# Optimization experiments

Measured on AMD Instinct MI355X. Metric: run time of the kernel, lower is better.

Reference implementation:

```python
import jax, jax.numpy as jnp
from jax import lax
import numpy as np


def _hsig(x):
    # Keras hard_sigmoid (default recurrent_activation of ConvLSTM2D)
    return jnp.clip(0.2 * x + 0.5, 0.0, 1.0)


def _conv(x, k):
    return lax.conv_general_dilated(x, k, (1, 1), 'SAME',
                                    dimension_numbers=('NHWC', 'HWIO', 'NHWC'))


def _convlstm(x, W, U, b, return_seq=True):
    # x: [B,T,H,W,Cin]; W: [kh,kw,Cin,4C]; U: [kh,kw,C,4C]; b: [4C]
    B, T, H, Wd, Ci = x.shape
    C = b.shape[0] // 4
    # input-to-gate convs for all timesteps at once (batched over B*T)
    xz = _conv(x.reshape(B * T, H, Wd, Ci), W).reshape(B, T, H, Wd, 4 * C) + b

    def step(carry, z_t):
        h, c = carry
        z = z_t + _conv(h, U)
        zi, zf, zc, zo = jnp.split(z, 4, axis=-1)  # Keras gate order i,f,c,o
        c = _hsig(zf) * c + _hsig(zi) * jax.nn.relu(zc)  # activation='relu'
        h = _hsig(zo) * jax.nn.relu(c)
        return (h, c), h

    h0 = jnp.zeros((B, H, Wd, C), x.dtype)
    (hT, _), hs = lax.scan(step, (h0, h0), jnp.swapaxes(xz, 0, 1))
    return jnp.swapaxes(hs, 0, 1) if return_seq else hT


def _pool(x):  # MaxPooling3D(pool_size=(1,2,2)) on [B,T,H,W,C]
    return lax.reduce_window(x, -jnp.inf, lax.max,
                             (1, 1, 2, 2, 1), (1, 1, 2, 2, 1), 'VALID')


def _up(x):  # UpSampling3D(size=(1,2,2))
    return jnp.repeat(jnp.repeat(x, 2, axis=2), 2, axis=3)


def _forward(x, w1a, u1a, b1a, w1b, u1b, b1b, w2a, u2a, b2a, w2b, u2b, b2b,
             w3a, u3a, b3a, w3b, u3b, b3b, w4a, u4a, b4a, w4b, u4b, b4b,
             w5a, u5a, b5a, w5b, u5b, b5b, w6a, u6a, b6a, w6b, u6b, b6b,
             w7a, u7a, b7a, w7b, u7b, b7b, wout, uout, bout):
    c1 = _convlstm(_convlstm(x, w1a, u1a, b1a), w1b, u1b, b1b)
    c2 = _convlstm(_convlstm(_pool(c1), w2a, u2a, b2a), w2b, u2b, b2b)
    c3 = _convlstm(_convlstm(_pool(c2), w3a, u3a, b3a), w3b, u3b, b3b)
    c4 = _convlstm(_convlstm(_pool(c3), w4a, u4a, b4a), w4b, u4b, b4b)
    m5 = jnp.concatenate([c3, _up(c4)], axis=-1)
    c5 = _convlstm(_convlstm(m5, w5a, u5a, b5a), w5b, u5b, b5b)
    m6 = jnp.concatenate([c2, _up(c5)], axis=-1)
    c6 = _convlstm(_convlstm(m6, w6a, u6a, b6a), w6b, u6b, b6b)
    m7 = jnp.concatenate([c1, _up(c6)], axis=-1)
    c7 = _convlstm(_convlstm(m7, w7a, u7a, b7a), w7b, u7b, b7b)
    return _convlstm(c7, wout, uout, bout, return_seq=False)  # [B,H,W,1]


def setup_inputs() -> dict:
    key = jax.random.key(0)
    keys = iter(jax.random.split(key, 64))

    def p(*s):
        return jax.random.normal(next(keys), s, jnp.float32) * 0.05

    d = {'x': jax.random.normal(next(keys), (1, 4, 256, 256, 1), jnp.float32)}
    specs = [('1a', 1, 32), ('1b', 32, 32), ('2a', 32, 64), ('2b', 64, 64),
             ('3a', 64, 128), ('3b', 128, 128), ('4a', 128, 256), ('4b', 256, 256),
             ('5a', 384, 128), ('5b', 128, 128), ('6a', 192, 64), ('6b', 64, 64),
             ('7a', 96, 32), ('7b', 32, 32)]
    for n, ci, co in specs:
        d['w' + n] = p(3, 3, ci, 4 * co)
        d['u' + n] = p(3, 3, co, 4 * co)
        d['b' + n] = jnp.zeros((4 * co,), jnp.float32)
    d['wout'] = p(1, 1, 32, 4)
    d['uout'] = p(1, 1, 1, 4)
    d['bout'] = jnp.zeros((4,), jnp.float32)
    return d


def reference(x, w1a, u1a, b1a, w1b, u1b, b1b, w2a, u2a, b2a, w2b, u2b, b2b,
              w3a, u3a, b3a, w3b, u3b, b3b, w4a, u4a, b4a, w4b, u4b, b4b,
              w5a, u5a, b5a, w5b, u5b, b5b, w6a, u6a, b6a, w6b, u6b, b6b,
              w7a, u7a, b7a, w7b, u7b, b7b, wout, uout, bout):
    return _forward(x, w1a, u1a, b1a, w1b, u1b, b1b, w2a, u2a, b2a, w2b, u2b, b2b,
                    w3a, u3a, b3a, w3b, u3b, b3b, w4a, u4a, b4a, w4b, u4b, b4b,
                    w5a, u5a, b5a, w5b, u5b, b5b, w6a, u6a, b6a, w6b, u6b, b6b,
                    w7a, u7a, b7a, w7b, u7b, b7b, wout, uout, bout)
```

## Files before the change

kernel.cpp:

```cpp
#include <hip/hip_runtime.h>
#include <hip/hip_bf16.h>

#define T_STEPS 4

typedef __attribute__((ext_vector_type(8))) short short8v;
typedef __attribute__((ext_vector_type(4))) float f32x4;
typedef __attribute__((ext_vector_type(4))) unsigned short us4;

__device__ __forceinline__ float hsig(float x) {
    return fminf(fmaxf(0.2f * x + 0.5f, 0.f), 1.f);
}
__device__ __forceinline__ unsigned short f2bf(float v) {
    __hip_bfloat16 h = __float2bfloat16(v);
    unsigned short u; __builtin_memcpy(&u, &h, 2); return u;
}

template<int TILE>
__global__ __launch_bounds__(256, (TILE == 16) ? 3 : 6)
void lstm_mfma(const float* __restrict__ xin, const float* __restrict__ hprev,
               float* __restrict__ cst, float* __restrict__ hout,
               const unsigned short* __restrict__ BtX,
               const unsigned short* __restrict__ BtH,
               const float* __restrict__ bias,
               int H, int W, int CiR, int CiP, int C)
{
    constexpr int HS = TILE + 2;
    constexpr int PITCH = 40;
    constexpr int NSLOT = HS * HS * 8;
    constexpr int NFM = (TILE == 16) ? 4 : 2;
    constexpr int NN  = (TILE == 16) ? 4 : 2;
    extern __shared__ char smem[];
    unsigned short* ldsA = (unsigned short*)smem;

    const int tid = threadIdx.x, w = tid >> 6, lane = tid & 63;
    const int nb = blockIdx.z;
    const int y0 = blockIdx.y * TILE, x0 = blockIdx.x * TILE;
    const int NG = (4 * C) >> 4;
    const int kq = lane >> 4;

    int abase;
    if (TILE == 16) abase = (w * 4) * HS * PITCH + (lane & 15) * PITCH + kq * 8;
    else abase = ((w >> 1) * 4 + ((lane >> 3) & 1)) * HS * PITCH + (lane & 7) * PITCH + kq * 8;

    f32x4 acc[NFM][NN];
#pragma unroll
    for (int a = 0; a < NFM; ++a)
#pragma unroll
        for (int b = 0; b < NN; ++b) acc[a][b] = (f32x4)0.f;

    for (int s = 0; s < 2; ++s) {
        if (s == 1 && hprev == nullptr) break;
        const float* __restrict__ src = s ? hprev : xin;
        const int CsR = s ? C : CiR;
        const int CsP = s ? C : CiP;
        const unsigned short* __restrict__ Bt = s ? BtH : BtX;
        const int nch = CsP >> 5;

        for (int ck = 0; ck < nch; ++ck) {
            __syncthreads();
            const int ci0 = ck << 5;
            for (int i = tid; i < NSLOT; i += 256) {
                const int pix = i >> 3, c4 = (i & 7) << 2;
                const int hy = pix / HS, hx = pix - hy * HS;
                const int iy = y0 + hy - 1, ix = x0 + hx - 1;
                float4 v = make_float4(0.f, 0.f, 0.f, 0.f);
                if (iy >= 0 && iy < H && ix >= 0 && ix < W) {
                    const float* gp = src + ((size_t)iy * W + ix) * CsR + ci0 + c4;
                    if (ci0 + c4 + 4 <= CsR) v = *(const float4*)gp;
                    else {
                        const int rem = CsR - ci0 - c4;
                        if (rem > 0) { v.x = gp[0]; if (rem > 1) v.y = gp[1]; if (rem > 2) v.z = gp[2]; }
                    }
                }
                us4 hi;
                hi[0] = f2bf(v.x); hi[1] = f2bf(v.y);
                hi[2] = f2bf(v.z); hi[3] = f2bf(v.w);
                *(us4*)(ldsA + pix * PITCH + c4) = hi;
            }
            short8v bcur[NN], bnxt[NN];
#pragma unroll
            for (int nn = 0; nn < NN; ++nn) {
                const int ng = (TILE == 16) ? nn : ((w & 1) * 2 + nn);
                bcur[nn] = *(const short8v*)(Bt +
                    ((size_t)((ck * 9) * NG + nb * 4 + ng) << 9) + lane * 8);
            }
            __syncthreads();
#pragma unroll
            for (int dd = 0; dd < 9; ++dd) {
                if (dd < 8) {
#pragma unroll
                    for (int nn = 0; nn < NN; ++nn) {
                        const int ng = (TILE == 16) ? nn : ((w & 1) * 2 + nn);
                        bnxt[nn] = *(const short8v*)(Bt +
                            ((size_t)((ck * 9 + dd + 1) * NG + nb * 4 + ng) << 9) + lane * 8);
                    }
                }
                const int dy = dd / 3, dx = dd % 3;
                short8v ah[NFM];
#pragma unroll
                for (int fm = 0; fm < NFM; ++fm) {
                    const int ro = (TILE == 16) ? (fm + dy) : (2 * fm + dy);
                    ah[fm] = *(const short8v*)(ldsA + abase + (ro * HS + dx) * PITCH);
                }
#pragma unroll
                for (int nn = 0; nn < NN; ++nn)
#pragma unroll
                    for (int fm = 0; fm < NFM; ++fm)
                        acc[fm][nn] = __builtin_amdgcn_mfma_f32_16x16x32_bf16(ah[fm], bcur[nn], acc[fm][nn], 0, 0, 0);
                if (dd < 8) {
#pragma unroll
                    for (int nn = 0; nn < NN; ++nn) bcur[nn] = bnxt[nn];
                }
            }
        }
    }

    __syncthreads();
    float* lds2 = (float*)smem + w * 276;
    const int rr = lane & 15, cl = lane >> 4;
#pragma unroll
    for (int nn = 0; nn < NN; ++nn) {
        const int ngl = (TILE == 16) ? nn : ((w & 1) * 2 + nn);
        const int c = nb * 16 + ngl * 4 + cl;
        float b4[4];
#pragma unroll
        for (int g = 0; g < 4; ++g) b4[g] = bias[g * C + c];
#pragma unroll
        for (int fm = 0; fm < NFM; ++fm) {
#pragma unroll
            for (int j = 0; j < 4; ++j) lds2[(cl * 4 + j) * 17 + rr] = acc[fm][nn][j];
            float z[4];
#pragma unroll
            for (int g = 0; g < 4; ++g) z[g] = lds2[rr * 17 + cl * 4 + g];
            int py, px;
            if (TILE == 16) { py = y0 + w * 4 + fm; px = x0 + rr; }
            else { py = y0 + (w >> 1) * 4 + 2 * fm + (rr >> 3); px = x0 + (rr & 7); }
            const size_t base = ((size_t)py * W + px) * C + c;
            const float cold = hprev ? cst[base] : 0.f;
            const float zi = z[0] + b4[0], zf = z[1] + b4[1];
            const float zc = z[2] + b4[2], zo = z[3] + b4[3];
            const float cn = hsig(zf) * cold + hsig(zi) * fmaxf(zc, 0.f);
            const float hv = hsig(zo) * fmaxf(cn, 0.f);
            cst[base] = cn; hout[base] = hv;
        }
    }
}

__global__ void transform_w_kernel(const float* __restrict__ Wsrc,
                                   unsigned short* __restrict__ Bt,
                                   int CsR, int C, int total)
{
    const int i = blockIdx.x * 256 + threadIdx.x;
    if (i >= total) return;
    const int N = 4 * C, NG = N >> 4;
    const int lane = i & 63; int t = i >> 6;
    const int ng = t % NG; t /= NG;
    const int dd = t % 9; const int ck = t / 9;
    const int colp = ng * 16 + (lane & 15);
    const int c = colp >> 2, g = colp & 3, co = g * C + c;
    const int kb = (lane >> 4) * 8;
    short8v hi8;
#pragma unroll
    for (int e = 0; e < 8; ++e) {
        const int ci = (ck << 5) + kb + e;
        const float v = (ci < CsR) ? Wsrc[(size_t)(dd * CsR + ci) * N + co] : 0.f;
        hi8[e] = (short)f2bf(v);
    }
    const size_t base = ((size_t)(ck * 9 + dd) * NG + ng) * 512 + lane * 8;
    *(short8v*)(Bt + base) = hi8;
}

__global__ void pool_kernel(const float* __restrict__ in, float* __restrict__ out,
                            int H, int Wd, int C, long total4)
{
    const int Ho = H >> 1, Wo = Wd >> 1;
    const int C4 = C >> 2;
    for (long i = (long)blockIdx.x * blockDim.x + threadIdx.x; i < total4;
         i += (long)gridDim.x * blockDim.x) {
        const int c4 = (int)(i % C4);
        long r = i / C4;
        const int x = (int)(r % Wo); r /= Wo;
        const int y = (int)(r % Ho);
        const int t = (int)(r / Ho);
        const float4* a = reinterpret_cast<const float4*>(in) +
                          (((long)t * H + 2 * y) * Wd + 2 * x) * C4 + c4;
        const float4 v00 = a[0], v01 = a[C4];
        const float4 v10 = a[(long)Wd * C4], v11 = a[(long)Wd * C4 + C4];
        float4 o;
        o.x = fmaxf(fmaxf(v00.x, v01.x), fmaxf(v10.x, v11.x));
        o.y = fmaxf(fmaxf(v00.y, v01.y), fmaxf(v10.y, v11.y));
        o.z = fmaxf(fmaxf(v00.z, v01.z), fmaxf(v10.z, v11.z));
        o.w = fmaxf(fmaxf(v00.w, v01.w), fmaxf(v10.w, v11.w));
        reinterpret_cast<float4*>(out)[i] = o;
    }
}

__global__ void upconcat_kernel(const float* __restrict__ A, const float* __restrict__ B,
                                float* __restrict__ out, int H, int Wd, int C1, int C2,
                                long total4)
{
    const int Co4 = (C1 + C2) >> 2, C14 = C1 >> 2, C24 = C2 >> 2;
    for (long i = (long)blockIdx.x * blockDim.x + threadIdx.x; i < total4;
         i += (long)gridDim.x * blockDim.x) {
        const int c4 = (int)(i % Co4);
        long r = i / Co4;
        const int x = (int)(r % Wd); r /= Wd;
        const int y = (int)(r % H);
        const int t = (int)(r / H);
        float4 v;
        if (c4 < C14)
            v = reinterpret_cast<const float4*>(A)[(((long)t * H + y) * Wd + x) * C14 + c4];
        else
            v = reinterpret_cast<const float4*>(B)[
                (((long)t * (H >> 1) + (y >> 1)) * (Wd >> 1) + (x >> 1)) * C24 + (c4 - C14)];
        reinterpret_cast<float4*>(out)[i] = v;
    }
}

__global__ void final_step_kernel(const float* __restrict__ h7, const float* __restrict__ hprev,
                                  float* __restrict__ cst, float* __restrict__ hout,
                                  const float* __restrict__ wout,
                                  const float* __restrict__ uout,
                                  const float* __restrict__ bout,
                                  float* __restrict__ dout, int N)
{
    const int i = blockIdx.x * 256 + threadIdx.x;
    if (i >= N) return;
    float z0 = bout[0], z1 = bout[1], z2 = bout[2], z3 = bout[3];
    const float* hp = h7 + (size_t)i * 32;
#pragma unroll
    for (int c = 0; c < 32; c += 4) {
        const float4 h4 = *reinterpret_cast<const float4*>(hp + c);
        const float hv4[4] = {h4.x, h4.y, h4.z, h4.w};
#pragma unroll
        for (int j = 0; j < 4; ++j) {
            z0 += hv4[j] * wout[(c + j) * 4 + 0];
            z1 += hv4[j] * wout[(c + j) * 4 + 1];
            z2 += hv4[j] * wout[(c + j) * 4 + 2];
            z3 += hv4[j] * wout[(c + j) * 4 + 3];
        }
    }
    float hpv = 0.f, cold = 0.f;
    if (hprev) { hpv = hprev[i]; cold = cst[i]; }
    z0 += hpv * uout[0]; z1 += hpv * uout[1]; z2 += hpv * uout[2]; z3 += hpv * uout[3];
    const float ig = hsig(z0), fg = hsig(z1), og = hsig(z3);
    const float cd = fmaxf(z2, 0.f);
    const float cn = fg * cold + ig * cd;
    const float hv = og * fmaxf(cn, 0.f);
    cst[i] = cn; hout[i] = hv;
    if (dout) dout[i] = hv;
}

struct LD { int H, W, CiR, CiP, C, tile, wi; };

static void run_layer(const LD& L, const float* in, float* out, float* cstate,
                      const unsigned short* btx, const unsigned short* bth,
                      const float* bias, hipStream_t stream)
{
    const size_t inS = (size_t)L.H * L.W * L.CiR, outS = (size_t)L.H * L.W * L.C;
    const dim3 grid(L.W / L.tile, L.H / L.tile, (4 * L.C) / 64);
    for (int t = 0; t < T_STEPS; ++t) {
        const float* hp = t ? out + (t - 1) * outS : nullptr;
        if (L.tile == 16) {
            const size_t sh = (size_t)18 * 18 * 40 * 2;
            lstm_mfma<16><<<grid, 256, sh, stream>>>(in + t * inS, hp, cstate, out + t * outS,
                                                     btx, bth, bias, L.H, L.W, L.CiR, L.CiP, L.C);
        } else {
            const size_t sh = (size_t)10 * 10 * 40 * 2;
            lstm_mfma<8><<<grid, 256, sh, stream>>>(in + t * inS, hp, cstate, out + t * outS,
                                                    btx, bth, bias, L.H, L.W, L.CiR, L.CiP, L.C);
        }
    }
}

extern "C" void kernel_launch(void* const* d_in, const int* in_sizes, int n_in,
                              void* d_out, int out_size, void* d_ws, size_t ws_size,
                              hipStream_t stream)
{
    (void)in_sizes; (void)n_in; (void)out_size; (void)ws_size;
    const float* x = (const float*)d_in[0];
    auto Wp = [&](int k) { return (const float*)d_in[k]; };
    char* ws = (char*)d_ws;
    const size_t MiB = 1ull << 20;
    auto f = [&](size_t m) { return (float*)(ws + m * MiB); };

    hipFuncSetAttribute((const void*)lstm_mfma<16>,
                        hipFuncAttributeMaxDynamicSharedMemorySize, 26624);
    hipFuncSetAttribute((const void*)lstm_mfma<8>,
                        hipFuncAttributeMaxDynamicSharedMemorySize, 8192);

    float* bC1  = f(0);    float* bC2  = f(32);  float* bC3  = f(48);
    float* bCST = f(56);
    float* bHF  = (float*)(ws + 64 * MiB);
    float* bCF  = (float*)(ws + 64 * MiB + 256 * 1024);
    float* bS1A = f(65);   float* bP1  = f(97);  float* bS2A = f(105);
    float* bP2  = f(97);   float* bS3A = f(101); float* bP3  = f(65);
    float* bS4A = f(67);   float* bC4  = f(71);  float* bM5  = f(75);
    float* bS5A = f(99);   float* bC5  = f(65);  float* bM6  = f(73);
    float* bS6A = f(121);  float* bC6  = f(65);  float* bM7  = f(81);
    float* bS7A = f(0);    float* bC7  = f(81);

    static const LD Ls[14] = {
        {256, 256,   1,  32,  32, 16,  1}, {256, 256,  32,  32,  32, 16,  4},
        {128, 128,  32,  32,  64,  8,  7}, {128, 128,  64,  64,  64,  8, 10},
        { 64,  64,  64,  64, 128,  8, 13}, { 64,  64, 128, 128, 128,  8, 16},
        { 32,  32, 128, 128, 256,  8, 19}, { 32,  32, 256, 256, 256,  8, 22},
        { 64,  64, 384, 384, 128,  8, 25}, { 64,  64, 128, 128, 128,  8, 28},
        {128, 128, 192, 192,  64,  8, 31}, {128, 128,  64,  64,  64,  8, 34},
        {256, 256,  96,  96,  32, 16, 37}, {256, 256,  32,  32,  32, 16, 40},
    };

    unsigned short* btx[14]; unsigned short* bth[14];
    {
        size_t cur = 177 * MiB;
        for (int i = 0; i < 14; ++i) {
            const LD& L = Ls[i];
            const int NG = (4 * L.C) >> 4;
            const size_t szx = (size_t)(L.CiP >> 5) * 9 * NG * 1024;
            const size_t szh = (size_t)(L.C  >> 5) * 9 * NG * 1024;
            btx[i] = (unsigned short*)(ws + cur); cur += szx;
            bth[i] = (unsigned short*)(ws + cur); cur += szh;
            const int totx = (L.CiP >> 5) * 9 * NG * 64;
            const int toth = (L.C  >> 5) * 9 * NG * 64;
            transform_w_kernel<<<(totx + 255) / 256, 256, 0, stream>>>(
                Wp(L.wi), btx[i], L.CiR, L.C, totx);
            transform_w_kernel<<<(toth + 255) / 256, 256, 0, stream>>>(
                Wp(L.wi + 1), bth[i], L.C, L.C, toth);
        }
    }

    auto pool = [&](const float* in, float* out, int H, int Wd, int C) {
        long total4 = (long)T_STEPS * (H / 2) * (Wd / 2) * (C / 4);
        long nb = (total4 + 255) / 256; if (nb > 4096) nb = 4096;
        pool_kernel<<<dim3((unsigned)nb), 256, 0, stream>>>(in, out, H, Wd, C, total4);
    };
    auto upcat = [&](const float* A, const float* B, float* out, int H, int Wd, int C1, int C2) {
        long total4 = (long)T_STEPS * H * Wd * ((C1 + C2) / 4);
        long nb = (total4 + 255) / 256; if (nb > 8192) nb = 8192;
        upconcat_kernel<<<dim3((unsigned)nb), 256, 0, stream>>>(A, B, out, H, Wd, C1, C2, total4);
    };
    auto run = [&](int i, const float* in, float* out) {
        run_layer(Ls[i], in, out, bCST, btx[i], bth[i], Wp(Ls[i].wi + 2), stream);
    };

    run(0, x, bS1A);        run(1, bS1A, bC1);
    pool(bC1, bP1, 256, 256, 32);
    run(2, bP1, bS2A);      run(3, bS2A, bC2);
    pool(bC2, bP2, 128, 128, 64);
    run(4, bP2, bS3A);      run(5, bS3A, bC3);
    pool(bC3, bP3, 64, 64, 128);
    run(6, bP3, bS4A);      run(7, bS4A, bC4);
    upcat(bC3, bC4, bM5, 64, 64, 128, 256);
    run(8, bM5, bS5A);      run(9, bS5A, bC5);
    upcat(bC2, bC5, bM6, 128, 128, 64, 128);
    run(10, bM6, bS6A);     run(11, bS6A, bC6);
    upcat(bC1, bC6, bM7, 256, 256, 32, 64);
    run(12, bM7, bS7A);     run(13, bS7A, bC7);

    const int N = 256 * 256;
    for (int t = 0; t < T_STEPS; ++t) {
        const float* h7 = bC7 + (size_t)t * N * 32;
        final_step_kernel<<<N / 256, 256, 0, stream>>>(
            h7, t ? bHF : nullptr, bCF, bHF, Wp(43), Wp(44), Wp(45),
            (t == T_STEPS - 1) ? (float*)d_out : nullptr, N);
    }
}
```

Baseline: 2.146 ms.

## Prefetch next input chunk into registers during MFMA loop; batch weight transforms

The main ConvLSTM kernel now merges the x and h channel-chunk loops into one loop. It issues the global loads for the next chunk into registers before running the current chunk's MFMAs, so load latency overlaps with compute. The LDS store only converts the staged values to bf16. This costs extra registers, so the launch-bounds occupancy targets are lowered. The 28 separate weight-transform launches are also combined into a single 2D-grid launch to cut launch overhead.

```diff
diff --git a/kernel.cpp b/kernel.cpp
--- a/kernel.cpp
+++ b/kernel.cpp
@@ -16,7 +16,7 @@
 }
 
 template<int TILE>
-__global__ __launch_bounds__(256, (TILE == 16) ? 3 : 6)
+__global__ __launch_bounds__(256, (TILE == 16) ? 2 : 4)
 void lstm_mfma(const float* __restrict__ xin, const float* __restrict__ hprev,
                float* __restrict__ cst, float* __restrict__ hout,
                const unsigned short* __restrict__ BtX,
@@ -27,6 +27,7 @@
     constexpr int HS = TILE + 2;
     constexpr int PITCH = 40;
     constexpr int NSLOT = HS * HS * 8;
+    constexpr int ITERS = (NSLOT + 255) / 256;
     constexpr int NFM = (TILE == 16) ? 4 : 2;
     constexpr int NN  = (TILE == 16) ? 4 : 2;
     extern __shared__ char smem[];
@@ -48,22 +49,23 @@
 #pragma unroll
         for (int b = 0; b < NN; ++b) acc[a][b] = (f32x4)0.f;
 
-    for (int s = 0; s < 2; ++s) {
-        if (s == 1 && hprev == nullptr) break;
-        const float* __restrict__ src = s ? hprev : xin;
-        const int CsR = s ? C : CiR;
-        const int CsP = s ? C : CiP;
-        const unsigned short* __restrict__ Bt = s ? BtH : BtX;
-        const int nch = CsP >> 5;
-
-        for (int ck = 0; ck < nch; ++ck) {
-            __syncthreads();
-            const int ci0 = ck << 5;
-            for (int i = tid; i < NSLOT; i += 256) {
+    const int nchx = CiP >> 5;
+    const int nchh = hprev ? (C >> 5) : 0;
+    const int NCH = nchx + nchh;
+
+    float4 stg[ITERS];
+    auto issue = [&](int t) {
+        const float* __restrict__ src = (t < nchx) ? xin : hprev;
+        const int CsR = (t < nchx) ? CiR : C;
+        const int ci0 = ((t < nchx) ? t : t - nchx) << 5;
+#pragma unroll
+        for (int it = 0; it < ITERS; ++it) {
+            const int i = tid + it * 256;
+            float4 v = make_float4(0.f, 0.f, 0.f, 0.f);
+            if (i < NSLOT) {
                 const int pix = i >> 3, c4 = (i & 7) << 2;
                 const int hy = pix / HS, hx = pix - hy * HS;
                 const int iy = y0 + hy - 1, ix = x0 + hx - 1;
-                float4 v = make_float4(0.f, 0.f, 0.f, 0.f);
                 if (iy >= 0 && iy < H && ix >= 0 && ix < W) {
                     const float* gp = src + ((size_t)iy * W + ix) * CsR + ci0 + c4;
                     if (ci0 + c4 + 4 <= CsR) v = *(const float4*)gp;
@@ -72,45 +74,61 @@
                         if (rem > 0) { v.x = gp[0]; if (rem > 1) v.y = gp[1]; if (rem > 2) v.z = gp[2]; }
                     }
                 }
+            }
+            stg[it] = v;
+        }
+    };
+
+    issue(0);
+    for (int t = 0; t < NCH; ++t) {
+        const unsigned short* __restrict__ Bt = (t < nchx) ? BtX : BtH;
+        const int bck = (t < nchx) ? t : t - nchx;
+        __syncthreads();
+#pragma unroll
+        for (int it = 0; it < ITERS; ++it) {
+            const int i = tid + it * 256;
+            if (i < NSLOT) {
+                const int pix = i >> 3, c4 = (i & 7) << 2;
                 us4 hi;
-                hi[0] = f2bf(v.x); hi[1] = f2bf(v.y);
-                hi[2] = f2bf(v.z); hi[3] = f2bf(v.w);
+                hi[0] = f2bf(stg[it].x); hi[1] = f2bf(stg[it].y);
+                hi[2] = f2bf(stg[it].z); hi[3] = f2bf(stg[it].w);
                 *(us4*)(ldsA + pix * PITCH + c4) = hi;
             }
-            short8v bcur[NN], bnxt[NN];
-#pragma unroll
-            for (int nn = 0; nn < NN; ++nn) {
-                const int ng = (TILE == 16) ? nn : ((w & 1) * 2 + nn);
-                bcur[nn] = *(const short8v*)(Bt +
-                    ((size_t)((ck * 9) * NG + nb * 4 + ng) << 9) + lane * 8);
-            }
-            __syncthreads();
-#pragma unroll
-            for (int dd = 0; dd < 9; ++dd) {
-                if (dd < 8) {
-#pragma unroll
-                    for (int nn = 0; nn < NN; ++nn) {
-                        const int ng = (TILE == 16) ? nn : ((w & 1) * 2 + nn);
-                        bnxt[nn] = *(const short8v*)(Bt +
-                            ((size_t)((ck * 9 + dd + 1) * NG + nb * 4 + ng) << 9) + lane * 8);
-                    }
+        }
+        __syncthreads();
+        short8v bcur[NN], bnxt[NN];
+#pragma unroll
+        for (int nn = 0; nn < NN; ++nn) {
+            const int ng = (TILE == 16) ? nn : ((w & 1) * 2 + nn);
+            bcur[nn] = *(const short8v*)(Bt +
+                ((size_t)((bck * 9) * NG + nb * 4 + ng) << 9) + lane * 8);
+        }
+        if (t + 1 < NCH) issue(t + 1);
+#pragma unroll
+        for (int dd = 0; dd < 9; ++dd) {
+            if (dd < 8) {
+#pragma unroll
+                for (int nn = 0; nn < NN; ++nn) {
+                    const int ng = (TILE == 16) ? nn : ((w & 1) * 2 + nn);
+                    bnxt[nn] = *(const short8v*)(Bt +
+                        ((size_t)((bck * 9 + dd + 1) * NG + nb * 4 + ng) << 9) + lane * 8);
                 }
-                const int dy = dd / 3, dx = dd % 3;
-                short8v ah[NFM];
-#pragma unroll
-                for (int fm = 0; fm < NFM; ++fm) {
-                    const int ro = (TILE == 16) ? (fm + dy) : (2 * fm + dy);
-                    ah[fm] = *(const short8v*)(ldsA + abase + (ro * HS + dx) * PITCH);
-                }
-#pragma unroll
-                for (int nn = 0; nn < NN; ++nn)
-#pragma unroll
-                    for (int fm = 0; fm < NFM; ++fm)
-                        acc[fm][nn] = __builtin_amdgcn_mfma_f32_16x16x32_bf16(ah[fm], bcur[nn], acc[fm][nn], 0, 0, 0);
-                if (dd < 8) {
-#pragma unroll
-                    for (int nn = 0; nn < NN; ++nn) bcur[nn] = bnxt[nn];
-                }
+            }
+            const int dy = dd / 3, dx = dd % 3;
+            short8v ah[NFM];
+#pragma unroll
+            for (int fm = 0; fm < NFM; ++fm) {
+                const int ro = (TILE == 16) ? (fm + dy) : (2 * fm + dy);
+                ah[fm] = *(const short8v*)(ldsA + abase + (ro * HS + dx) * PITCH);
+            }
+#pragma unroll
+            for (int nn = 0; nn < NN; ++nn)
+#pragma unroll
+                for (int fm = 0; fm < NFM; ++fm)
+                    acc[fm][nn] = __builtin_amdgcn_mfma_f32_16x16x32_bf16(ah[fm], bcur[nn], acc[fm][nn], 0, 0, 0);
+            if (dd < 8) {
+#pragma unroll
+                for (int nn = 0; nn < NN; ++nn) bcur[nn] = bnxt[nn];
             }
         }
     }
@@ -146,28 +164,30 @@
     }
 }
 
-__global__ void transform_w_kernel(const float* __restrict__ Wsrc,
-                                   unsigned short* __restrict__ Bt,
-                                   int CsR, int C, int total)
-{
+struct TJob { const float* src; unsigned short* dst; int CsR; int C; int total; };
+struct TJobs { TJob j[28]; };
+
+__global__ void transform_all_kernel(TJobs jobs)
+{
+    const TJob J = jobs.j[blockIdx.y];
     const int i = blockIdx.x * 256 + threadIdx.x;
-    if (i >= total) return;
-    const int N = 4 * C, NG = N >> 4;
+    if (i >= J.total) return;
+    const int N = 4 * J.C, NG = N >> 4;
     const int lane = i & 63; int t = i >> 6;
     const int ng = t % NG; t /= NG;
     const int dd = t % 9; const int ck = t / 9;
     const int colp = ng * 16 + (lane & 15);
-    const int c = colp >> 2, g = colp & 3, co = g * C + c;
+    const int c = colp >> 2, g = colp & 3, co = g * J.C + c;
     const int kb = (lane >> 4) * 8;
     short8v hi8;
 #pragma unroll
     for (int e = 0; e < 8; ++e) {
         const int ci = (ck << 5) + kb + e;
-        const float v = (ci < CsR) ? Wsrc[(size_t)(dd * CsR + ci) * N + co] : 0.f;
+        const float v = (ci < J.CsR) ? J.src[(size_t)(dd * J.CsR + ci) * N + co] : 0.f;
         hi8[e] = (short)f2bf(v);
     }
     const size_t base = ((size_t)(ck * 9 + dd) * NG + ng) * 512 + lane * 8;
-    *(short8v*)(Bt + base) = hi8;
+    *(short8v*)(J.dst + base) = hi8;
 }
 
 __global__ void pool_kernel(const float* __restrict__ in, float* __restrict__ out,
@@ -312,6 +332,8 @@
 
     unsigned short* btx[14]; unsigned short* bth[14];
     {
+        TJobs jobs;
+        int maxTotal = 0;
         size_t cur = 177 * MiB;
         for (int i = 0; i < 14; ++i) {
             const LD& L = Ls[i];
@@ -322,11 +344,12 @@
             bth[i] = (unsigned short*)(ws + cur); cur += szh;
             const int totx = (L.CiP >> 5) * 9 * NG * 64;
             const int toth = (L.C  >> 5) * 9 * NG * 64;
-            transform_w_kernel<<<(totx + 255) / 256, 256, 0, stream>>>(
-                Wp(L.wi), btx[i], L.CiR, L.C, totx);
-            transform_w_kernel<<<(toth + 255) / 256, 256, 0, stream>>>(
-                Wp(L.wi + 1), bth[i], L.C, L.C, toth);
-        }
+            jobs.j[2 * i]     = {Wp(L.wi),     btx[i], L.CiR, L.C, totx};
+            jobs.j[2 * i + 1] = {Wp(L.wi + 1), bth[i], L.C,   L.C, toth};
+            if (totx > maxTotal) maxTotal = totx;
+            if (toth > maxTotal) maxTotal = toth;
+        }
+        transform_all_kernel<<<dim3((maxTotal + 255) / 256, 28), 256, 0, stream>>>(jobs);
     }
 
     auto pool = [&](const float* in, float* out, int H, int Wd, int C) {
```

New measurement: 1.830 ms. -14.7%, faster.
